# Optimization experiments

Measured on AMD Instinct MI355X. Metric: run time of the kernel, lower is better.

The kernel has to match this reference:

```python
import jax, jax.numpy as jnp
import numpy as np

N = 8192
DIM_A = 512
DIM_B = 512
HID = 64
MOTIVE = 64


def setup_inputs() -> dict:
    key = jax.random.key(0)
    ks = jax.random.split(key, 10)
    s = lambda fan_in: 1.0 / np.sqrt(fan_in)
    return {
        "X_A": jax.random.normal(ks[0], (N, DIM_A), jnp.float32),
        "X_B": jax.random.normal(ks[1], (N, DIM_B), jnp.float32),
        "WA1": jax.random.uniform(ks[2], (DIM_A, HID), jnp.float32, -s(DIM_A), s(DIM_A)),
        "bA1": jnp.zeros((HID,), jnp.float32),
        "WA2": jax.random.uniform(ks[3], (HID, MOTIVE), jnp.float32, -s(HID), s(HID)),
        "bA2": jnp.zeros((MOTIVE,), jnp.float32),
        "WB1": jax.random.uniform(ks[4], (DIM_B, HID), jnp.float32, -s(DIM_B), s(DIM_B)),
        "bB1": jnp.zeros((HID,), jnp.float32),
        "WB2": jax.random.uniform(ks[5], (HID, MOTIVE), jnp.float32, -s(HID), s(HID)),
        "bB2": jnp.zeros((MOTIVE,), jnp.float32),
    }


def _functor(x, W1, b1, W2, b2):
    return jax.nn.relu(x @ W1 + b1) @ W2 + b2


def _sq_cdist(x, y):
    # squared euclidean distance matrix [N, N]; clamp for numerical safety
    xx = jnp.sum(x * x, axis=-1)[:, None]
    yy = jnp.sum(y * y, axis=-1)[None, :]
    return jnp.maximum(xx + yy - 2.0 * (x @ y.T), 0.0)


def reference(X_A, X_B, WA1, bA1, WA2, bA2, WB1, bB1, WB2, bB2):
    M_A = _functor(X_A, WA1, bA1, WA2, bA2)  # [N, motive_dim]
    M_B = _functor(X_B, WB1, bB1, WB2, bB2)
    sigma = 1.0
    inv = 1.0 / (2.0 * sigma ** 2)
    k_xx = jnp.exp(-_sq_cdist(M_A, M_A) * inv).mean()
    k_yy = jnp.exp(-_sq_cdist(M_B, M_B) * inv).mean()
    k_xy = jnp.exp(-_sq_cdist(M_A, M_B) * inv).mean()
    mmd_loss = k_xx + k_yy - 2.0 * k_xy
    return (mmd_loss, M_A, M_B)
```

## Files before the change

kernel.cpp:

```cpp
#include <hip/hip_runtime.h>
#include <hip/hip_bf16.h>
#include <cstdint>
#include <cstddef>

#define N_ROWS 8192
#define DIM_IN 512
#define MOT 64
#define INV_N2 (1.0f / (8192.0f * 8192.0f))
#define PAIR_BLOCKS 1024

typedef __attribute__((ext_vector_type(8))) short bf16x8;
typedef __attribute__((ext_vector_type(4))) float f32x4;

#define HALF_L2E 0.721347520444481703f

__device__ inline float fast_exp2(float x) {
    return __builtin_amdgcn_exp2f(x);
}

__device__ inline unsigned short f2bf(float f) {
    union { __hip_bfloat16 h; unsigned short u; } cv;
    cv.h = __float2bfloat16(f);
    return cv.u;
}
__device__ inline float bfbits2f(unsigned short u) {
    union { unsigned int i; float f; } cv;
    cv.i = ((unsigned int)u) << 16;
    return cv.f;
}

__global__ __launch_bounds__(256) void functor2_kernel(
    const float* __restrict__ XA, const float* __restrict__ WA1, const float* __restrict__ bA1,
    const float* __restrict__ WA2, const float* __restrict__ bA2,
    const float* __restrict__ XB, const float* __restrict__ WB1, const float* __restrict__ bB1,
    const float* __restrict__ WB2, const float* __restrict__ bB2,
    float* __restrict__ MA, float* __restrict__ MB,
    float* __restrict__ nAo, float* __restrict__ nBo,
    unsigned short* __restrict__ PbfA, unsigned short* __restrict__ PbfB)
{
    const int half = blockIdx.x >> 8;
    const float* X  = half ? XB  : XA;
    const float* W1 = half ? WB1 : WA1;
    const float* b1 = half ? bB1 : bA1;
    const float* W2 = half ? WB2 : WA2;
    const float* b2 = half ? bB2 : bA2;
    float* Mout  = half ? MB  : MA;
    float* norms = half ? nBo : nAo;
    unsigned short* Pbf = half ? PbfB : PbfA;

    __shared__ float XsT[64][34];
    __shared__ float Ws[64][64];
    __shared__ float HsT[64][34];

    const int t  = threadIdx.x;
    const int tx = t & 15;
    const int ty = t >> 4;
    const int row0 = (blockIdx.x & 255) * 32;

    float c[2][4] = {};

    for (int kc = 0; kc < DIM_IN; kc += 64) {
        #pragma unroll
        for (int q = 0; q < 2; ++q) {
            int idx = q * 256 + t;
            int row = idx >> 4;
            int k4  = (idx & 15) << 2;
            float4 v = *(const float4*)&X[(size_t)(row0 + row) * DIM_IN + kc + k4];
            XsT[k4 + 0][row] = v.x;
            XsT[k4 + 1][row] = v.y;
            XsT[k4 + 2][row] = v.z;
            XsT[k4 + 3][row] = v.w;
        }
        #pragma unroll
        for (int q = 0; q < 4; ++q) {
            int idx = q * 256 + t;
            int row = idx >> 4;
            int k4  = (idx & 15) << 2;
            *(float4*)&Ws[row][k4] = *(const float4*)&W1[(size_t)(kc + row) * MOT + k4];
        }
        __syncthreads();
        #pragma unroll 8
        for (int k = 0; k < 64; ++k) {
            float2 a = *(const float2*)&XsT[k][ty * 2];
            float4 b = *(const float4*)&Ws[k][tx * 4];
            float av[2] = {a.x, a.y};
            float bv[4] = {b.x, b.y, b.z, b.w};
            #pragma unroll
            for (int i = 0; i < 2; ++i)
                #pragma unroll
                for (int j = 0; j < 4; ++j)
                    c[i][j] = fmaf(av[i], bv[j], c[i][j]);
        }
        __syncthreads();
    }

    {
        float bias1[4];
        #pragma unroll
        for (int j = 0; j < 4; ++j) bias1[j] = b1[tx * 4 + j];
        #pragma unroll
        for (int i = 0; i < 2; ++i)
            #pragma unroll
            for (int j = 0; j < 4; ++j) {
                float h = c[i][j] + bias1[j];
                HsT[tx * 4 + j][ty * 2 + i] = fmaxf(h, 0.0f);
                c[i][j] = 0.0f;
            }
    }

    #pragma unroll
    for (int q = 0; q < 4; ++q) {
        int idx = q * 256 + t;
        int row = idx >> 4;
        int k4  = (idx & 15) << 2;
        *(float4*)&Ws[row][k4] = *(const float4*)&W2[(size_t)row * MOT + k4];
    }
    __syncthreads();

    #pragma unroll 8
    for (int k = 0; k < 64; ++k) {
        float2 a = *(const float2*)&HsT[k][ty * 2];
        float4 b = *(const float4*)&Ws[k][tx * 4];
        float av[2] = {a.x, a.y};
        float bv[4] = {b.x, b.y, b.z, b.w};
        #pragma unroll
        for (int i = 0; i < 2; ++i)
            #pragma unroll
            for (int j = 0; j < 4; ++j)
                c[i][j] = fmaf(av[i], bv[j], c[i][j]);
    }

    float bias2[4];
    #pragma unroll
    for (int j = 0; j < 4; ++j) bias2[j] = b2[tx * 4 + j];

    float p[2] = {0.0f, 0.0f};
    #pragma unroll
    for (int i = 0; i < 2; ++i) {
        unsigned short q4[4];
        int grow = row0 + ty * 2 + i;
        #pragma unroll
        for (int j = 0; j < 4; ++j) {
            float m = c[i][j] + bias2[j];
            Mout[(size_t)grow * MOT + tx * 4 + j] = m;
            q4[j] = f2bf(m);
            float mn = bfbits2f(q4[j]);
            p[i] = fmaf(mn, mn, p[i]);
        }
        int r = grow & 127;
        size_t tile = (size_t)(grow >> 7);
        int swz = (tx * 8) ^ ((r & 7) << 4);
        ushort4 v; v.x = q4[0]; v.y = q4[1]; v.z = q4[2]; v.w = q4[3];
        *(ushort4*)((char*)Pbf + tile * 16384 + (size_t)r * 128 + swz) = v;
    }
    #pragma unroll
    for (int off = 1; off < 16; off <<= 1)
        #pragma unroll
        for (int i = 0; i < 2; ++i)
            p[i] += __shfl_xor(p[i], off, 64);
    if (tx == 0) {
        norms[row0 + ty * 2 + 0] = HALF_L2E * p[0];
        norms[row0 + ty * 2 + 1] = HALF_L2E * p[1];
    }
}

__device__ inline void decode_tile(int id, int T, int TRI, int& which, int& bi, int& bj) {
    if (id < 2 * TRI) {
        which = (id < TRI) ? 0 : 1;
        if (which) id -= TRI;
        int r = (int)((sqrtf(8.0f * (float)id + 1.0f) - 1.0f) * 0.5f);
        while ((r + 1) * (r + 2) / 2 <= id) ++r;
        while (r * (r + 1) / 2 > id) --r;
        bi = r;
        bj = id - r * (r + 1) / 2;
    } else {
        id -= 2 * TRI;
        which = 2;
        bi = id >> 6;
        bj = id & (T - 1);
    }
}

__device__ inline void step_tile(int& which, int& bi, int& bj, int T) {
    ++bj;
    if (which == 2) {
        if (bj == T) { bj = 0; ++bi; }
    } else {
        if (bj > bi) { bj = 0; ++bi; if (bi == T) { bi = 0; ++which; } }
    }
}

__global__ __launch_bounds__(256, 4) void pair_v6_kernel(
    const unsigned short* __restrict__ PA, const unsigned short* __restrict__ PB,
    const float* __restrict__ nA, const float* __restrict__ nB,
    float* __restrict__ out0)
{
    const int T   = N_ROWS / 128;
    const int TRI = T * (T + 1) / 2;
    const float L2E = 1.44269504088896341f;

    __shared__ float red[4];

    const int t    = threadIdx.x;
    const int lane = t & 63;
    const int wave = t >> 6;
    const int wr   = wave >> 1, wc = wave & 1;
    const int sw   = (lane & 7) << 4;
    const int kb   = (lane >> 4) << 4;

    const int b     = blockIdx.x;
    const int start = (b < 64) ? b * 9 : b * 8 + 64;
    const int len   = (b < 64) ? 9 : 8;

    bf16x8 af[4][2];
    float  nAr[4][4];

    auto loadA = [&](int w_, int bi_) {
        const unsigned short* P = (w_ == 1) ? PB : PA;
        const float* nP         = (w_ == 1) ? nB : nA;
        const char* base = (const char*)P + (size_t)bi_ * 16384;
        #pragma unroll
        for (int i = 0; i < 4; ++i) {
            const char* rowp = base + (size_t)(wr * 64 + i * 16 + (lane & 15)) * 128;
            #pragma unroll
            for (int k0 = 0; k0 < 2; ++k0)
                af[i][k0] = *(const bf16x8*)(rowp + ((k0 * 64 + kb) ^ sw));
            float4 n4 = *(const float4*)&nP[bi_ * 128 + wr * 64 + i * 16 + ((lane >> 4) << 2)];
            nAr[i][0] = n4.x; nAr[i][1] = n4.y; nAr[i][2] = n4.z; nAr[i][3] = n4.w;
        }
    };

    int cw, cbi, cbj;
    decode_tile(start, T, TRI, cw, cbi, cbj);
    loadA(cw, cbi);

    float s_acc = 0.0f;

    for (int u = 0; u < len; ++u) {
        const unsigned short* Q = (cw == 0) ? PA : PB;
        const float* nQ         = (cw == 0) ? nA : nB;
        const char* bbase = (const char*)Q + (size_t)cbj * 16384;
        const bool diag = (cw != 2) && (cbi == cbj);

        float sa[4] = {0.0f, 0.0f, 0.0f, 0.0f};

        #pragma unroll
        for (int jh = 0; jh < 2; ++jh) {
            f32x4 acc[4][2] = {};
            #pragma unroll
            for (int k0 = 0; k0 < 2; ++k0) {
                const int koff = (k0 * 64 + kb) ^ sw;
                bf16x8 bfr[2];
                #pragma unroll
                for (int j = 0; j < 2; ++j)
                    bfr[j] = *(const bf16x8*)(bbase +
                        (size_t)(wc * 64 + jh * 32 + j * 16 + (lane & 15)) * 128 + koff);
                #pragma unroll
                for (int i = 0; i < 4; ++i)
                    #pragma unroll
                    for (int j = 0; j < 2; ++j)
                        acc[i][j] = __builtin_amdgcn_mfma_f32_16x16x32_bf16(af[i][k0], bfr[j], acc[i][j], 0, 0, 0);
            }

            float posB[2];
            #pragma unroll
            for (int j = 0; j < 2; ++j)
                posB[j] = nQ[cbj * 128 + wc * 64 + jh * 32 + j * 16 + (lane & 15)];

            if (diag) {
                #pragma unroll
                for (int i = 0; i < 4; ++i)
                    #pragma unroll
                    for (int j = 0; j < 2; ++j)
                        #pragma unroll
                        for (int r = 0; r < 4; ++r) {
                            float tv = fmaf(acc[i][j][r], L2E, -nAr[i][r]) - posB[j];
                            sa[jh * 2 + j] += fast_exp2(fminf(tv, 0.0f));
                        }
            } else {
                #pragma unroll
                for (int i = 0; i < 4; ++i)
                    #pragma unroll
                    for (int j = 0; j < 2; ++j)
                        #pragma unroll
                        for (int r = 0; r < 4; ++r) {
                            float tv = fmaf(acc[i][j][r], L2E, -nAr[i][r]) - posB[j];
                            sa[jh * 2 + j] += fast_exp2(tv);
                        }
            }
        }

        float stile = (sa[0] + sa[1]) + (sa[2] + sa[3]);
        float scale = (cw == 2) ? (-2.0f * INV_N2)
                                : ((cbi != cbj) ? (2.0f * INV_N2) : INV_N2);
        s_acc = fmaf(scale, stile, s_acc);

        if (u + 1 < len) {
            int nw = cw, nbi = cbi, nbj = cbj;
            step_tile(nw, nbi, nbj, T);
            if (nw != cw || nbi != cbi) loadA(nw, nbi);
            cw = nw; cbi = nbi; cbj = nbj;
        }
    }

    #pragma unroll
    for (int off = 32; off > 0; off >>= 1) s_acc += __shfl_xor(s_acc, off, 64);
    if (lane == 0) red[wave] = s_acc;
    __syncthreads();
    if (t == 0) atomicAdd(out0, red[0] + red[1] + red[2] + red[3]);
}

extern "C" void kernel_launch(void* const* d_in, const int* in_sizes, int n_in,
                              void* d_out, int out_size, void* d_ws, size_t ws_size,
                              hipStream_t stream)
{
    const float* XA  = (const float*)d_in[0];
    const float* XB  = (const float*)d_in[1];
    const float* WA1 = (const float*)d_in[2];
    const float* bA1 = (const float*)d_in[3];
    const float* WA2 = (const float*)d_in[4];
    const float* bA2 = (const float*)d_in[5];
    const float* WB1 = (const float*)d_in[6];
    const float* bB1 = (const float*)d_in[7];
    const float* WB2 = (const float*)d_in[8];
    const float* bB2 = (const float*)d_in[9];

    float* out = (float*)d_out;
    float* MA  = out + 1;
    float* MB  = out + 1 + (size_t)N_ROWS * MOT;
    float* nA  = (float*)d_ws;
    float* nB  = nA + N_ROWS;
    unsigned short* PA = (unsigned short*)(nB + N_ROWS);
    unsigned short* PB = PA + (size_t)N_ROWS * MOT;

    hipMemsetAsync(d_out, 0, sizeof(float), stream);

    functor2_kernel<<<512, 256, 0, stream>>>(XA, WA1, bA1, WA2, bA2,
                                             XB, WB1, bB1, WB2, bB2,
                                             MA, MB, nA, nB, PA, PB);

    pair_v6_kernel<<<PAIR_BLOCKS, 256, 0, stream>>>(PA, PB, nA, nB, out);
}
```

Measured before the change: 71.68 us.

## Software-pipeline B-fragment loads across 16-column passes and next tile

Restructures the pair kernel's inner loop into four 16-column passes that use double-buffered B fragments. Each pass prefetches the next pass's B data, and the last pass prefetches the next tile's first fragment, its norms and its A fragments, so global load latency overlaps MFMA and exp work. It also applies the fminf clamp to every tile, removing the diag branch, and hoists the swizzled offsets. In exchange it uses more registers under the 4-waves launch bound and has smaller MFMA batches per pass.

```diff
diff --git a/kernel.cpp b/kernel.cpp
--- a/kernel.cpp
+++ b/kernel.cpp
@@ -190,7 +190,7 @@
     }
 }
 
-__global__ __launch_bounds__(256, 4) void pair_v6_kernel(
+__global__ __launch_bounds__(256, 4) void pair_v7_kernel(
     const unsigned short* __restrict__ PA, const unsigned short* __restrict__ PB,
     const float* __restrict__ nA, const float* __restrict__ nB,
     float* __restrict__ out0)
@@ -207,6 +207,8 @@
     const int wr   = wave >> 1, wc = wave & 1;
     const int sw   = (lane & 7) << 4;
     const int kb   = (lane >> 4) << 4;
+    const int koff0 = kb ^ sw;
+    const int koff1 = (64 + kb) ^ sw;
 
     const int b     = blockIdx.x;
     const int start = (b < 64) ? b * 9 : b * 8 + 64;
@@ -222,86 +224,98 @@
         #pragma unroll
         for (int i = 0; i < 4; ++i) {
             const char* rowp = base + (size_t)(wr * 64 + i * 16 + (lane & 15)) * 128;
-            #pragma unroll
-            for (int k0 = 0; k0 < 2; ++k0)
-                af[i][k0] = *(const bf16x8*)(rowp + ((k0 * 64 + kb) ^ sw));
+            af[i][0] = *(const bf16x8*)(rowp + koff0);
+            af[i][1] = *(const bf16x8*)(rowp + koff1);
             float4 n4 = *(const float4*)&nP[bi_ * 128 + wr * 64 + i * 16 + ((lane >> 4) << 2)];
             nAr[i][0] = n4.x; nAr[i][1] = n4.y; nAr[i][2] = n4.z; nAr[i][3] = n4.w;
         }
+    };
+
+    auto loadB = [&](bf16x8 (&buf)[2], const char* bb, int jq) {
+        const char* colp = bb + (size_t)((wc << 6) + (jq << 4) + (lane & 15)) * 128;
+        buf[0] = *(const bf16x8*)(colp + koff0);
+        buf[1] = *(const bf16x8*)(colp + koff1);
     };
 
     int cw, cbi, cbj;
     decode_tile(start, T, TRI, cw, cbi, cbj);
     loadA(cw, cbi);
 
+    const char* bbase;
+    const float* nQ;
+    {
+        const unsigned short* Q = (cw == 0) ? PA : PB;
+        nQ    = (cw == 0) ? nA : nB;
+        bbase = (const char*)Q + (size_t)cbj * 16384;
+    }
+
+    bf16x8 bufE[2], bufO[2];
+    loadB(bufE, bbase, 0);
+
+    float posB[4];
+    #pragma unroll
+    for (int jq = 0; jq < 4; ++jq)
+        posB[jq] = nQ[cbj * 128 + (wc << 6) + (jq << 4) + (lane & 15)];
+
     float s_acc = 0.0f;
 
+#define PASS(JQ, BCUR, PREFETCH)                                                                  \
+    {                                                                                             \
+        f32x4 acc[4] = {};                                                                        \
+        _Pragma("unroll")                                                                         \
+        for (int i = 0; i < 4; ++i)                                                               \
+            acc[i] = __builtin_amdgcn_mfma_f32_16x16x32_bf16(af[i][0], BCUR[0], acc[i], 0, 0, 0); \
+        _Pragma("unroll")                                                                         \
+        for (int i = 0; i < 4; ++i)                                                               \
+            acc[i] = __builtin_amdgcn_mfma_f32_16x16x32_bf16(af[i][1], BCUR[1], acc[i], 0, 0, 0); \
+        PREFETCH;                                                                                 \
+        _Pragma("unroll")                                                                         \
+        for (int i = 0; i < 4; ++i)                                                               \
+            _Pragma("unroll")                                                                     \
+            for (int r = 0; r < 4; ++r) {                                                         \
+                float tv = fmaf(acc[i][r], L2E, -nAr[i][r]) - posB[JQ];                           \
+                sa[JQ] += fast_exp2(fminf(tv, 0.0f));                                             \
+            }                                                                                     \
+    }
+
     for (int u = 0; u < len; ++u) {
-        const unsigned short* Q = (cw == 0) ? PA : PB;
-        const float* nQ         = (cw == 0) ? nA : nB;
-        const char* bbase = (const char*)Q + (size_t)cbj * 16384;
-        const bool diag = (cw != 2) && (cbi == cbj);
+        const bool have = (u + 1 < len);
+        int nw = cw, nbi = cbi, nbj = cbj;
+        if (have) step_tile(nw, nbi, nbj, T);
+        const unsigned short* nQp = (nw == 0) ? PA : PB;
+        const float* nnQ          = (nw == 0) ? nA : nB;
+        const char* nbbase        = (const char*)nQp + (size_t)nbj * 16384;
 
         float sa[4] = {0.0f, 0.0f, 0.0f, 0.0f};
-
-        #pragma unroll
-        for (int jh = 0; jh < 2; ++jh) {
-            f32x4 acc[4][2] = {};
-            #pragma unroll
-            for (int k0 = 0; k0 < 2; ++k0) {
-                const int koff = (k0 * 64 + kb) ^ sw;
-                bf16x8 bfr[2];
-                #pragma unroll
-                for (int j = 0; j < 2; ++j)
-                    bfr[j] = *(const bf16x8*)(bbase +
-                        (size_t)(wc * 64 + jh * 32 + j * 16 + (lane & 15)) * 128 + koff);
-                #pragma unroll
-                for (int i = 0; i < 4; ++i)
-                    #pragma unroll
-                    for (int j = 0; j < 2; ++j)
-                        acc[i][j] = __builtin_amdgcn_mfma_f32_16x16x32_bf16(af[i][k0], bfr[j], acc[i][j], 0, 0, 0);
+        float4 npb;
+
+        PASS(0, bufE, { loadB(bufO, bbase, 1); })
+        PASS(1, bufO, { loadB(bufE, bbase, 2); })
+        PASS(2, bufE, { loadB(bufO, bbase, 3); })
+        PASS(3, bufO, {
+            if (have) {
+                loadB(bufE, nbbase, 0);
+                const int cb = (wc << 6) + (lane & 15);
+                npb.x = nnQ[nbj * 128 + cb];
+                npb.y = nnQ[nbj * 128 + cb + 16];
+                npb.z = nnQ[nbj * 128 + cb + 32];
+                npb.w = nnQ[nbj * 128 + cb + 48];
+                if (nw != cw || nbi != cbi) loadA(nw, nbi);
             }
-
-            float posB[2];
-            #pragma unroll
-            for (int j = 0; j < 2; ++j)
-                posB[j] = nQ[cbj * 128 + wc * 64 + jh * 32 + j * 16 + (lane & 15)];
-
-            if (diag) {
-                #pragma unroll
-                for (int i = 0; i < 4; ++i)
-                    #pragma unroll
-                    for (int j = 0; j < 2; ++j)
-                        #pragma unroll
-                        for (int r = 0; r < 4; ++r) {
-                            float tv = fmaf(acc[i][j][r], L2E, -nAr[i][r]) - posB[j];
-                            sa[jh * 2 + j] += fast_exp2(fminf(tv, 0.0f));
-                        }
-            } else {
-                #pragma unroll
-                for (int i = 0; i < 4; ++i)
-                    #pragma unroll
-                    for (int j = 0; j < 2; ++j)
-                        #pragma unroll
-                        for (int r = 0; r < 4; ++r) {
-                            float tv = fmaf(acc[i][j][r], L2E, -nAr[i][r]) - posB[j];
-                            sa[jh * 2 + j] += fast_exp2(tv);
-                        }
-            }
-        }
+        })
 
         float stile = (sa[0] + sa[1]) + (sa[2] + sa[3]);
         float scale = (cw == 2) ? (-2.0f * INV_N2)
                                 : ((cbi != cbj) ? (2.0f * INV_N2) : INV_N2);
         s_acc = fmaf(scale, stile, s_acc);
 
-        if (u + 1 < len) {
-            int nw = cw, nbi = cbi, nbj = cbj;
-            step_tile(nw, nbi, nbj, T);
-            if (nw != cw || nbi != cbi) loadA(nw, nbi);
+        if (have) {
+            posB[0] = npb.x; posB[1] = npb.y; posB[2] = npb.z; posB[3] = npb.w;
             cw = nw; cbi = nbi; cbj = nbj;
-        }
-    }
+            bbase = nbbase;
+        }
+    }
+#undef PASS
 
     #pragma unroll
     for (int off = 32; off > 0; off >>= 1) s_acc += __shfl_xor(s_acc, off, 64);
@@ -339,5 +353,5 @@
                                              XB, WB1, bB1, WB2, bB2,
                                              MA, MB, nA, nB, PA, PB);
 
-    pair_v6_kernel<<<PAIR_BLOCKS, 256, 0, stream>>>(PA, PB, nA, nB, out);
-}
+    pair_v7_kernel<<<PAIR_BLOCKS, 256, 0, stream>>>(PA, PB, nA, nB, out);
+}
```

After: 131.0 us. 1.83x slower.

## Double-buffer B tiles in LDS via async global_load_lds prefetch

Applied to the files above, without the earlier changes.

The pair kernel now stages each B tile (16 KB of bf16 packed rows plus its 128 norms) into a double-buffered LDS region using direct global-to-LDS loads. The next tile is prefetched while the current tile is computed, and MFMA operands are read from LDS instead of straight from global memory. The diagonal/off-diagonal branch is merged into one path that always clamps the exponent. This adds a __syncthreads per tile and about 33 KB of LDS per block, which could limit occupancy below the 4-blocks hint. The barrier that guards the buffer refill also relies on synchronization of the async loads.

```diff
diff --git a/kernel.cpp b/kernel.cpp
--- a/kernel.cpp
+++ b/kernel.cpp
@@ -27,6 +27,16 @@
     union { unsigned int i; float f; } cv;
     cv.i = ((unsigned int)u) << 16;
     return cv.f;
+}
+__device__ inline void gl_lds16(const void* g, void* l) {
+    __builtin_amdgcn_global_load_lds(
+        (const __attribute__((address_space(1))) unsigned int*)g,
+        (__attribute__((address_space(3))) unsigned int*)l, 16, 0, 0);
+}
+__device__ inline void gl_lds4(const void* g, void* l) {
+    __builtin_amdgcn_global_load_lds(
+        (const __attribute__((address_space(1))) unsigned int*)g,
+        (__attribute__((address_space(3))) unsigned int*)l, 4, 0, 0);
 }
 
 __global__ __launch_bounds__(256) void functor2_kernel(
@@ -190,7 +200,7 @@
     }
 }
 
-__global__ __launch_bounds__(256, 4) void pair_v6_kernel(
+__global__ __launch_bounds__(256, 4) void pair_v9_kernel(
     const unsigned short* __restrict__ PA, const unsigned short* __restrict__ PB,
     const float* __restrict__ nA, const float* __restrict__ nB,
     float* __restrict__ out0)
@@ -199,6 +209,8 @@
     const int TRI = T * (T + 1) / 2;
     const float L2E = 1.44269504088896341f;
 
+    __shared__ unsigned short Bs[2][8192];
+    __shared__ float nBsh[2][128];
     __shared__ float red[4];
 
     const int t    = threadIdx.x;
@@ -230,18 +242,39 @@
         }
     };
 
+    auto stageB = [&](int nb, int w_, int bj_) {
+        const unsigned short* Q = (w_ == 0) ? PA : PB;
+        const float* nQ         = (w_ == 0) ? nA : nB;
+        const char* src = (const char*)Q + (size_t)bj_ * 16384 + wave * 1024 + lane * 16;
+        char* dst = (char*)&Bs[nb][0] + wave * 1024;
+        #pragma unroll
+        for (int p4 = 0; p4 < 4; ++p4)
+            gl_lds16(src + p4 * 4096, dst + p4 * 4096);
+        if (wave == 0) {
+            gl_lds4(&nQ[bj_ * 128 + lane],      &nBsh[nb][0]);
+            gl_lds4(&nQ[bj_ * 128 + 64 + lane], &nBsh[nb][64]);
+        }
+    };
+
     int cw, cbi, cbj;
     decode_tile(start, T, TRI, cw, cbi, cbj);
     loadA(cw, cbi);
+    stageB(0, cw, cbj);
 
     float s_acc = 0.0f;
 
     for (int u = 0; u < len; ++u) {
-        const unsigned short* Q = (cw == 0) ? PA : PB;
-        const float* nQ         = (cw == 0) ? nA : nB;
-        const char* bbase = (const char*)Q + (size_t)cbj * 16384;
-        const bool diag = (cw != 2) && (cbi == cbj);
-
+        const int cur = u & 1;
+        __syncthreads();
+
+        const bool have = (u + 1 < len);
+        int nw = cw, nbi = cbi, nbj = cbj;
+        if (have) {
+            step_tile(nw, nbi, nbj, T);
+            stageB(cur ^ 1, nw, nbj);
+        }
+
+        const char* Bb = (const char*)&Bs[cur][0];
         float sa[4] = {0.0f, 0.0f, 0.0f, 0.0f};
 
         #pragma unroll
@@ -253,7 +286,7 @@
                 bf16x8 bfr[2];
                 #pragma unroll
                 for (int j = 0; j < 2; ++j)
-                    bfr[j] = *(const bf16x8*)(bbase +
+                    bfr[j] = *(const bf16x8*)(Bb +
                         (size_t)(wc * 64 + jh * 32 + j * 16 + (lane & 15)) * 128 + koff);
                 #pragma unroll
                 for (int i = 0; i < 4; ++i)
@@ -265,29 +298,17 @@
             float posB[2];
             #pragma unroll
             for (int j = 0; j < 2; ++j)
-                posB[j] = nQ[cbj * 128 + wc * 64 + jh * 32 + j * 16 + (lane & 15)];
-
-            if (diag) {
+                posB[j] = nBsh[cur][wc * 64 + jh * 32 + j * 16 + (lane & 15)];
+
+            #pragma unroll
+            for (int i = 0; i < 4; ++i)
                 #pragma unroll
-                for (int i = 0; i < 4; ++i)
+                for (int j = 0; j < 2; ++j)
                     #pragma unroll
-                    for (int j = 0; j < 2; ++j)
-                        #pragma unroll
-                        for (int r = 0; r < 4; ++r) {
-                            float tv = fmaf(acc[i][j][r], L2E, -nAr[i][r]) - posB[j];
-                            sa[jh * 2 + j] += fast_exp2(fminf(tv, 0.0f));
-                        }
-            } else {
-                #pragma unroll
-                for (int i = 0; i < 4; ++i)
-                    #pragma unroll
-                    for (int j = 0; j < 2; ++j)
-                        #pragma unroll
-                        for (int r = 0; r < 4; ++r) {
-                            float tv = fmaf(acc[i][j][r], L2E, -nAr[i][r]) - posB[j];
-                            sa[jh * 2 + j] += fast_exp2(tv);
-                        }
-            }
+                    for (int r = 0; r < 4; ++r) {
+                        float tv = fmaf(acc[i][j][r], L2E, -nAr[i][r]) - posB[j];
+                        sa[jh * 2 + j] += fast_exp2(fminf(tv, 0.0f));
+                    }
         }
 
         float stile = (sa[0] + sa[1]) + (sa[2] + sa[3]);
@@ -295,9 +316,7 @@
                                 : ((cbi != cbj) ? (2.0f * INV_N2) : INV_N2);
         s_acc = fmaf(scale, stile, s_acc);
 
-        if (u + 1 < len) {
-            int nw = cw, nbi = cbi, nbj = cbj;
-            step_tile(nw, nbi, nbj, T);
+        if (have) {
             if (nw != cw || nbi != cbi) loadA(nw, nbi);
             cw = nw; cbi = nbi; cbj = nbj;
         }
@@ -339,5 +358,5 @@
                                              XB, WB1, bB1, WB2, bB2,
                                              MA, MB, nA, nB, PA, PB);
 
-    pair_v6_kernel<<<PAIR_BLOCKS, 256, 0, stream>>>(PA, PB, nA, nB, out);
-}
+    pair_v9_kernel<<<PAIR_BLOCKS, 256, 0, stream>>>(PA, PB, nA, nB, out);
+}
```

Result: slower. 120.3 us (+67.9%).
